# Kernel optimization log

Measured on AMD Instinct MI355X. Metric: run time of the kernel, lower is better.

The kernel has to match this reference:

```python
import jax, jax.numpy as jnp
import numpy as np

S, H = 8192, 2048


def setup_inputs() -> dict:
    key = jax.random.key(0)
    k1, k2, k3, k4, k5 = jax.random.split(key, 5)
    encoder_outputs = jax.random.normal(k1, (S, 1, H), dtype=jnp.float32)
    hidden = jax.random.normal(k2, (H,), dtype=jnp.float32)
    # nn.Linear(2H, H): weight [H, 2H], bias [H]
    lim = 1.0 / np.sqrt(2 * H)
    W_att = jax.random.uniform(k3, (H, 2 * H), dtype=jnp.float32, minval=-lim, maxval=lim)
    b_att = jax.random.uniform(k4, (H,), dtype=jnp.float32, minval=-lim, maxval=lim)
    w = jax.random.normal(k5, (1, H), dtype=jnp.float32)
    return {"encoder_outputs": encoder_outputs, "hidden": hidden,
            "W_att": W_att, "b_att": b_att, "w": w}


def reference(encoder_outputs, hidden, W_att, b_att, w):
    # Original loops over source_len: score_i = w . (Linear(cat(hidden, enc_i)))
    # Vectorized: build [S, 2H] once, one GEMM, one dot, one softmax.
    enc = encoder_outputs[:, 0, :]                      # [S, H]
    h = jnp.broadcast_to(hidden[None, :], enc.shape)    # [S, H]
    x = jnp.concatenate([h, enc], axis=1)               # [S, 2H]
    res = x @ W_att.T + b_att                           # [S, H]
    scores = res @ w[0]                                 # [S]
    attn = jax.nn.softmax(scores, axis=0)               # softmax over source_len
    return attn[None, None, :]                          # [1, 1, S]
```

## Files before the change

### kernel.cpp

```cpp
#include <hip/hip_runtime.h>
#include <math.h>

#define SS 8192
#define HH 2048
#define NBLK 256
#define NTHR 512

__device__ unsigned g_ctr = 0;
__device__ unsigned g_rel = 0;
__device__ float g_part[NBLK][HH];
__device__ float g_v2[HH];
__device__ unsigned long long g_pair[NBLK];

__device__ __forceinline__ void grid_barrier() {
    __syncthreads();
    if (threadIdx.x == 0) {
        unsigned old = __hip_atomic_fetch_add(&g_ctr, 1u, __ATOMIC_RELAXED,
                                              __HIP_MEMORY_SCOPE_AGENT);
        unsigned epoch = old / NBLK;
        if (old % NBLK == NBLK - 1u) {
            __hip_atomic_store(&g_rel, epoch + 1u, __ATOMIC_RELAXED,
                               __HIP_MEMORY_SCOPE_AGENT);
        } else {
            while (__hip_atomic_load(&g_rel, __ATOMIC_RELAXED,
                                     __HIP_MEMORY_SCOPE_AGENT) <= epoch)
                __builtin_amdgcn_s_sleep(8);
        }
    }
    asm volatile("" ::: "memory");
    __syncthreads();
}

__global__ __launch_bounds__(NTHR, 2) void fused_kernel(
    const float* __restrict__ enc,
    const float* __restrict__ W,
    const float* __restrict__ w,
    float* __restrict__ out)
{
    const int b    = blockIdx.x;
    const int t    = threadIdx.x;
    const int wave = t >> 6;
    const int lane = t & 63;

    __shared__ float v2s[HH];
    __shared__ float srow[32];
    __shared__ float mv[NBLK];
    __shared__ float sv[NBLK];
    __shared__ float red[2];

    {
        const int row0 = b * 8;
        const float4* base =
            (const float4*)(W + (size_t)row0 * (2 * HH) + HH) + t;
        float4 acc = {0.f, 0.f, 0.f, 0.f};
#pragma unroll
        for (int j = 0; j < 8; ++j) {
            float4 a = base[(size_t)j * ((2 * HH) / 4)];
            float wj = w[row0 + j];
            acc.x += wj * a.x; acc.y += wj * a.y;
            acc.z += wj * a.z; acc.w += wj * a.w;
        }
        float* dst = &g_part[b][t * 4];
        __hip_atomic_store(dst + 0, acc.x, __ATOMIC_RELAXED, __HIP_MEMORY_SCOPE_AGENT);
        __hip_atomic_store(dst + 1, acc.y, __ATOMIC_RELAXED, __HIP_MEMORY_SCOPE_AGENT);
        __hip_atomic_store(dst + 2, acc.z, __ATOMIC_RELAXED, __HIP_MEMORY_SCOPE_AGENT);
        __hip_atomic_store(dst + 3, acc.w, __ATOMIC_RELAXED, __HIP_MEMORY_SCOPE_AGENT);
    }

    grid_barrier();

    {
        const int c = b * 8 + wave;
        float s = 0.0f;
#pragma unroll
        for (int k = 0; k < 4; ++k)
            s += __hip_atomic_load(&g_part[lane + k * 64][c],
                                   __ATOMIC_RELAXED, __HIP_MEMORY_SCOPE_AGENT);
#pragma unroll
        for (int off = 32; off > 0; off >>= 1)
            s += __shfl_down(s, off);
        if (lane == 0)
            __hip_atomic_store(&g_v2[c], s, __ATOMIC_RELAXED,
                               __HIP_MEMORY_SCOPE_AGENT);
    }

    grid_barrier();

#pragma unroll
    for (int k = 0; k < 4; ++k)
        v2s[t + k * 512] = __hip_atomic_load(&g_v2[t + k * 512],
                                             __ATOMIC_RELAXED,
                                             __HIP_MEMORY_SCOPE_AGENT);
    __syncthreads();
    {
        const float4* v4 = (const float4*)v2s;
        float4 vf[8];
#pragma unroll
        for (int i = 0; i < 8; ++i) vf[i] = v4[lane + i * 64];

        const int row_base = b * 32 + wave * 4;
#pragma unroll
        for (int rr = 0; rr < 4; ++rr) {
            const int row = row_base + rr;
            const float4* e = (const float4*)(enc + (size_t)row * HH);
            float acc = 0.0f;
#pragma unroll
            for (int i = 0; i < 8; ++i) {
                float4 a = e[lane + i * 64];
                acc += a.x * vf[i].x + a.y * vf[i].y
                     + a.z * vf[i].z + a.w * vf[i].w;
            }
#pragma unroll
            for (int off = 32; off > 0; off >>= 1)
                acc += __shfl_down(acc, off);
            if (lane == 0) srow[wave * 4 + rr] = acc;
        }
    }
    __syncthreads();

    if (wave == 0) {
        float v = (lane < 32) ? srow[lane] : -INFINITY;
        float m = v;
#pragma unroll
        for (int off = 1; off < 64; off <<= 1)
            m = fmaxf(m, __shfl_xor(m, off));
        float s = (lane < 32) ? __expf(v - m) : 0.0f;
#pragma unroll
        for (int off = 1; off < 64; off <<= 1)
            s += __shfl_xor(s, off);
        if (lane == 0) {
            unsigned long long p =
                ((unsigned long long)__float_as_uint(s) << 32) |
                (unsigned long long)__float_as_uint(m);
            __hip_atomic_store(&g_pair[b], p, __ATOMIC_RELAXED,
                               __HIP_MEMORY_SCOPE_AGENT);
        }
    }

    grid_barrier();

    if (t < NBLK) {
        unsigned long long p = __hip_atomic_load(&g_pair[t], __ATOMIC_RELAXED,
                                                 __HIP_MEMORY_SCOPE_AGENT);
        mv[t] = __uint_as_float((unsigned)(p & 0xffffffffu));
        sv[t] = __uint_as_float((unsigned)(p >> 32));
    }
    __syncthreads();
    if (wave == 0) {
        float m4 = fmaxf(fmaxf(mv[lane], mv[lane + 64]),
                         fmaxf(mv[lane + 128], mv[lane + 192]));
#pragma unroll
        for (int off = 32; off > 0; off >>= 1)
            m4 = fmaxf(m4, __shfl_xor(m4, off));
        if (lane == 0) red[0] = m4;
    }
    __syncthreads();
    const float M = red[0];
    if (wave == 0) {
        float s4 = sv[lane]       * __expf(mv[lane]       - M)
                 + sv[lane + 64]  * __expf(mv[lane + 64]  - M)
                 + sv[lane + 128] * __expf(mv[lane + 128] - M)
                 + sv[lane + 192] * __expf(mv[lane + 192] - M);
#pragma unroll
        for (int off = 32; off > 0; off >>= 1)
            s4 += __shfl_xor(s4, off);
        if (lane == 0) red[1] = s4;
    }
    __syncthreads();
    const float inv = 1.0f / red[1];

    if (t < 32)
        out[b * 32 + t] = __expf(srow[t] - M) * inv;
}

extern "C" void kernel_launch(void* const* d_in, const int* in_sizes, int n_in,
                              void* d_out, int out_size, void* d_ws, size_t ws_size,
                              hipStream_t stream) {
    const float* enc   = (const float*)d_in[0];
    const float* W_att = (const float*)d_in[2];
    const float* w     = (const float*)d_in[4];

    float* out = (float*)d_out;

    hipLaunchKernelGGL(fused_kernel, dim3(NBLK), dim3(NTHR), 0, stream,
                       enc, W_att, w, out);
}
```

Measured before the change: 142.4 us.

## Prefetch W and encoder rows before barriers, reduce v2 via atomics, drop a barrier

Loads of the W slice and of each block's encoder rows are issued up front into registers, so the encoder read overlaps the first grid barrier instead of following it. The partial v2 reduction now uses atomicAdd into four spread copies of a double-buffered scratch array; every block then sums those four copies itself, which removes one grid barrier and the g_v2 round trip. Scratch is re-zeroed at the end of each launch, with the parity derived from the barrier counter. The cost is heavy register pressure (about 160 floats per thread for the encoder rows), atomic contention and non-deterministic summation order.

Result: faster. 138.1 us (-3.1%).

```diff
diff --git a/kernel.cpp b/kernel.cpp
--- a/kernel.cpp
+++ b/kernel.cpp
@@ -5,11 +5,11 @@
 #define HH 2048
 #define NBLK 256
 #define NTHR 512
+#define NP 4
 
 __device__ unsigned g_ctr = 0;
 __device__ unsigned g_rel = 0;
-__device__ float g_part[NBLK][HH];
-__device__ float g_v2[HH];
+__device__ float g_part[2][NP][HH] = {};
 __device__ unsigned long long g_pair[NBLK];
 
 __device__ __forceinline__ void grid_barrier() {
@@ -47,68 +47,76 @@
     __shared__ float mv[NBLK];
     __shared__ float sv[NBLK];
     __shared__ float red[2];
+    __shared__ unsigned sh_par;
+
+    if (t == 0) {
+        unsigned c = __hip_atomic_load(&g_ctr, __ATOMIC_RELAXED,
+                                       __HIP_MEMORY_SCOPE_AGENT);
+        sh_par = (c / (2u * NBLK)) & 1u;
+    }
+    __syncthreads();
+    const unsigned par = sh_par;
+
+    const int row0 = b * 8;
+    const float4* wbase =
+        (const float4*)(W + (size_t)row0 * (2 * HH) + HH) + t;
+    float4 wv[8];
+#pragma unroll
+    for (int j = 0; j < 8; ++j)
+        wv[j] = wbase[(size_t)j * ((2 * HH) / 4)];
+
+    const int rbase = b * 32 + wave * 4;
+    float4 er[4][8];
+#pragma unroll
+    for (int rr = 0; rr < 4; ++rr) {
+        const float4* e = (const float4*)(enc + (size_t)(rbase + rr) * HH);
+#pragma unroll
+        for (int i = 0; i < 8; ++i)
+            er[rr][i] = e[lane + i * 64];
+    }
 
     {
-        const int row0 = b * 8;
-        const float4* base =
-            (const float4*)(W + (size_t)row0 * (2 * HH) + HH) + t;
         float4 acc = {0.f, 0.f, 0.f, 0.f};
 #pragma unroll
         for (int j = 0; j < 8; ++j) {
-            float4 a = base[(size_t)j * ((2 * HH) / 4)];
             float wj = w[row0 + j];
-            acc.x += wj * a.x; acc.y += wj * a.y;
-            acc.z += wj * a.z; acc.w += wj * a.w;
-        }
-        float* dst = &g_part[b][t * 4];
-        __hip_atomic_store(dst + 0, acc.x, __ATOMIC_RELAXED, __HIP_MEMORY_SCOPE_AGENT);
-        __hip_atomic_store(dst + 1, acc.y, __ATOMIC_RELAXED, __HIP_MEMORY_SCOPE_AGENT);
-        __hip_atomic_store(dst + 2, acc.z, __ATOMIC_RELAXED, __HIP_MEMORY_SCOPE_AGENT);
-        __hip_atomic_store(dst + 3, acc.w, __ATOMIC_RELAXED, __HIP_MEMORY_SCOPE_AGENT);
+            acc.x += wj * wv[j].x; acc.y += wj * wv[j].y;
+            acc.z += wj * wv[j].z; acc.w += wj * wv[j].w;
+        }
+        float* dst = &g_part[par][b & 3][t * 4];
+        atomicAdd(dst + 0, acc.x);
+        atomicAdd(dst + 1, acc.y);
+        atomicAdd(dst + 2, acc.z);
+        atomicAdd(dst + 3, acc.w);
     }
 
     grid_barrier();
 
-    {
-        const int c = b * 8 + wave;
+#pragma unroll
+    for (int k = 0; k < 4; ++k) {
+        const int c = t + k * 512;
         float s = 0.0f;
 #pragma unroll
-        for (int k = 0; k < 4; ++k)
-            s += __hip_atomic_load(&g_part[lane + k * 64][c],
-                                   __ATOMIC_RELAXED, __HIP_MEMORY_SCOPE_AGENT);
-#pragma unroll
-        for (int off = 32; off > 0; off >>= 1)
-            s += __shfl_down(s, off);
-        if (lane == 0)
-            __hip_atomic_store(&g_v2[c], s, __ATOMIC_RELAXED,
-                               __HIP_MEMORY_SCOPE_AGENT);
-    }
-
-    grid_barrier();
-
-#pragma unroll
-    for (int k = 0; k < 4; ++k)
-        v2s[t + k * 512] = __hip_atomic_load(&g_v2[t + k * 512],
-                                             __ATOMIC_RELAXED,
-                                             __HIP_MEMORY_SCOPE_AGENT);
-    __syncthreads();
+        for (int p = 0; p < NP; ++p)
+            s += __hip_atomic_load(&g_part[par][p][c], __ATOMIC_RELAXED,
+                                   __HIP_MEMORY_SCOPE_AGENT);
+        v2s[c] = s;
+    }
+    __syncthreads();
+
     {
         const float4* v4 = (const float4*)v2s;
         float4 vf[8];
 #pragma unroll
         for (int i = 0; i < 8; ++i) vf[i] = v4[lane + i * 64];
 
-        const int row_base = b * 32 + wave * 4;
 #pragma unroll
         for (int rr = 0; rr < 4; ++rr) {
-            const int row = row_base + rr;
-            const float4* e = (const float4*)(enc + (size_t)row * HH);
             float acc = 0.0f;
 #pragma unroll
             for (int i = 0; i < 8; ++i) {
-                float4 a = e[lane + i * 64];
-                acc += a.x * vf[i].x + a.y * vf[i].y
-                     + a.z * vf[i].z + a.w * vf[i].w;
+                acc += er[rr][i].x * vf[i].x + er[rr][i].y * vf[i].y
+                     + er[rr][i].z * vf[i].z + er[rr][i].w * vf[i].w;
             }
 #pragma unroll
             for (int off = 32; off > 0; off >>= 1)
@@ -139,6 +147,12 @@
 
     grid_barrier();
 
+    if (t < 32) {
+        const int idx = b * 32 + t;
+        __hip_atomic_store(&g_part[par][idx >> 11][idx & 2047], 0.0f,
+                           __ATOMIC_RELAXED, __HIP_MEMORY_SCOPE_AGENT);
+    }
+
     if (t < NBLK) {
         unsigned long long p = __hip_atomic_load(&g_pair[t], __ATOMIC_RELAXED,
                                                  __HIP_MEMORY_SCOPE_AGENT);
```
